# Optimization experiments

Hardware: AMD Instinct MI355X
Metric: run time of the kernel (lower is better)

## Reference

```python
import jax, jax.numpy as jnp
import numpy as np

H, KVH, DH = 16, 4, 128
EPS = 1e-8

def _rmsnorm(t, gamma):
    # normalize over last dim (dim_head)
    ms = jnp.mean(t * t, axis=-1, keepdims=True)
    return t * jax.lax.rsqrt(ms + EPS) * gamma

def setup_inputs() -> dict:
    key = jax.random.key(0)
    ks = jax.random.split(key, 5)
    d = H * DH  # 2048
    kv_d = KVH * DH  # 512
    x = jax.random.normal(ks[0], (2, 2048, d), dtype=jnp.float32)
    Wq = jax.random.normal(ks[1], (d, d), dtype=jnp.float32) * (d ** -0.5)
    Wk = jax.random.normal(ks[2], (d, kv_d), dtype=jnp.float32) * (d ** -0.5)
    Wv = jax.random.normal(ks[3], (d, kv_d), dtype=jnp.float32) * (d ** -0.5)
    Wo = jax.random.normal(ks[4], (d, d), dtype=jnp.float32) * (d ** -0.5)
    q_gamma = jnp.ones((DH,), dtype=jnp.float32)
    k_gamma = jnp.ones((DH,), dtype=jnp.float32)
    return {"x": x, "Wq": Wq, "Wk": Wk, "Wv": Wv, "Wo": Wo,
            "q_gamma": q_gamma, "k_gamma": k_gamma}

def reference(x, Wq, Wk, Wv, Wo, q_gamma, k_gamma):
    b, s, d = x.shape
    g = H // KVH  # GQA group size
    q = (x @ Wq).reshape(b, s, H, DH)
    k = (x @ Wk).reshape(b, s, KVH, DH)
    v = (x @ Wv).reshape(b, s, KVH, DH)
    # fused QK RMSNorm (per-head, over dim_head)
    q = _rmsnorm(q, q_gamma)
    k = _rmsnorm(k, k_gamma)
    # GQA: expand kv heads across query-head groups
    k = jnp.repeat(k, g, axis=2)  # [b, s, H, DH]
    v = jnp.repeat(v, g, axis=2)
    scores = jnp.einsum('bqhd,bkhd->bhqk', q, k) * (DH ** -0.5)
    causal = jnp.tril(jnp.ones((s, s), dtype=bool))
    scores = jnp.where(causal, scores, jnp.finfo(scores.dtype).min)
    attn = jax.nn.softmax(scores, axis=-1)
    out = jnp.einsum('bhqk,bkhd->bqhd', attn, v).reshape(b, s, H * DH)
    out = out @ Wo
    return out + x  # residual skip
```

## Files before the change

kernel.cpp:

```cpp
#include <hip/hip_runtime.h>

typedef unsigned short u16;
typedef __attribute__((ext_vector_type(8))) short short8;
typedef __attribute__((ext_vector_type(4))) float f32x4;

#define DEVI __device__ __forceinline__

DEVI float u2f(u16 u) {
    unsigned int x = ((unsigned int)u) << 16;
    float f; __builtin_memcpy(&f, &x, 4); return f;
}
DEVI u16 f2u(float f) {
    unsigned int x; __builtin_memcpy(&x, &f, 4);
    x = (x + 0x7fffu + ((x >> 16) & 1u)) >> 16;
    return (u16)x;
}
DEVI unsigned int fbits(float f) {
    unsigned int x; __builtin_memcpy(&x, &f, 4); return x;
}
DEVI void gld16(const u16* g, u16* ldsbase) {
    __builtin_amdgcn_global_load_lds(
        (const __attribute__((address_space(1))) unsigned int*)g,
        (__attribute__((address_space(3))) unsigned int*)ldsbase, 16, 0, 0);
}

__global__ __launch_bounds__(256) void prep(
    const float* __restrict__ x,
    const float* __restrict__ Wq, const float* __restrict__ Wk,
    const float* __restrict__ Wv, const float* __restrict__ Wo,
    u16* __restrict__ xbf, u16* __restrict__ WTqkv, u16* __restrict__ WoT)
{
    __shared__ u16 T[64 * 72];
    int id = blockIdx.x;
    const int tid = threadIdx.x;
    if (id < 4096) {
        int g = (id * 256 + tid) * 8;
        float4 a = *(const float4*)&x[g];
        float4 c = *(const float4*)&x[g + 4];
        short8 v;
        v[0]=(short)f2u(a.x); v[1]=(short)f2u(a.y); v[2]=(short)f2u(a.z); v[3]=(short)f2u(a.w);
        v[4]=(short)f2u(c.x); v[5]=(short)f2u(c.y); v[6]=(short)f2u(c.z); v[7]=(short)f2u(c.w);
        *(short8*)&xbf[g] = v;
        return;
    }
    id -= 4096;
    const float* W; u16* WT; int N, bx, by;
    if (id < 1024)      {            W = Wo; WT = WoT;   N = 2048; bx = id & 31; by = id >> 5; }
    else if (id < 2048) { id -= 1024; W = Wq; WT = WTqkv; N = 2048; bx = id & 31; by = id >> 5; }
    else if (id < 2304) { id -= 2048; W = Wk; WT = WTqkv + (size_t)2048 * 2048; N = 512; bx = id & 7; by = id >> 3; }
    else                { id -= 2304; W = Wv; WT = WTqkv + (size_t)2560 * 2048; N = 512; bx = id & 7; by = id >> 3; }
    const int K = 2048;
    const int k0 = by * 64, n0 = bx * 64;
#pragma unroll
    for (int i = 0; i < 2; ++i) {
        int c = tid + i * 256;
        int row = c >> 3, n8 = (c & 7) * 8;
        const float* src = &W[(size_t)(k0 + row) * N + n0 + n8];
#pragma unroll
        for (int j = 0; j < 8; ++j)
            T[(n8 + j) * 72 + row] = f2u(src[j]);
    }
    __syncthreads();
#pragma unroll
    for (int i = 0; i < 2; ++i) {
        int c = tid + i * 256;
        int n = c >> 3, k8 = (c & 7) * 8;
        *(short8*)&WT[(size_t)(n0 + n) * K + k0 + k8] = *(const short8*)&T[n * 72 + k8];
    }
}

__global__ __launch_bounds__(256) void gemm_lds(
    const u16* __restrict__ A, int lda,
    const u16* __restrict__ WT,
    void* __restrict__ C, int ldc, const float* __restrict__ resid, int c_f32,
    int M, int N, int K,
    const float* __restrict__ qg, const float* __restrict__ kg, int fuse_norm)
{
    __shared__ u16 As[128 * 32];
    __shared__ u16 Bs[128 * 32];
    const int tid = threadIdx.x;
    const int lane = tid & 63, w = tid >> 6;
    const int wm = w >> 1, wn = w & 1;
    const int l15 = lane & 15, quad = lane >> 4;
    const int r4 = lane >> 2, c4 = (lane & 3) * 8;
    const int m0 = blockIdx.y * 128, n0 = blockIdx.x * 128;

    f32x4 acc[4][4] = {};
    for (int k0 = 0; k0 < K; k0 += 32) {
#pragma unroll
        for (int j = 0; j < 2; ++j) {
            int row = w * 32 + j * 16;
            gld16(&WT[(size_t)(n0 + row + r4) * K + k0 + c4], &Bs[row * 32]);
            gld16(&A [(size_t)(m0 + row + r4) * lda + k0 + c4], &As[row * 32]);
        }
        __syncthreads();
        short8 a[4], b[4];
#pragma unroll
        for (int mt = 0; mt < 4; ++mt)
            a[mt] = *(const short8*)&As[(wm * 64 + mt * 16 + l15) * 32 + quad * 8];
#pragma unroll
        for (int nt = 0; nt < 4; ++nt)
            b[nt] = *(const short8*)&Bs[(wn * 64 + nt * 16 + l15) * 32 + quad * 8];
#pragma unroll
        for (int mt = 0; mt < 4; ++mt)
#pragma unroll
            for (int nt = 0; nt < 4; ++nt)
                acc[mt][nt] = __builtin_amdgcn_mfma_f32_16x16x32_bf16(a[mt], b[nt], acc[mt][nt], 0, 0, 0);
        __syncthreads();
    }

    if (fuse_norm && n0 < 2560) {
        const float* gamma = (n0 < 2048) ? qg : kg;
        float* red = (float*)As;
#pragma unroll
        for (int mt = 0; mt < 4; ++mt)
#pragma unroll
            for (int r = 0; r < 4; ++r) {
                float p = 0.f;
#pragma unroll
                for (int nt = 0; nt < 4; ++nt) p += acc[mt][nt][r] * acc[mt][nt][r];
#pragma unroll
                for (int msk = 1; msk < 16; msk <<= 1) p += __shfl_xor(p, msk);
                if (l15 == 0)
                    red[(wm * 64 + mt * 16 + quad * 4 + r) * 2 + wn] = p;
            }
        __syncthreads();
        float gv[4];
#pragma unroll
        for (int nt = 0; nt < 4; ++nt) gv[nt] = gamma[wn * 64 + nt * 16 + l15];
#pragma unroll
        for (int mt = 0; mt < 4; ++mt)
#pragma unroll
            for (int r = 0; r < 4; ++r) {
                int rl = wm * 64 + mt * 16 + quad * 4 + r;
                float m2 = red[rl * 2] + red[rl * 2 + 1];
                float sc = rsqrtf(m2 * (1.0f / 128.0f) + 1e-8f);
#pragma unroll
                for (int nt = 0; nt < 4; ++nt) acc[mt][nt][r] *= sc * gv[nt];
            }
    }

#pragma unroll
    for (int mt = 0; mt < 4; ++mt) {
#pragma unroll
        for (int r = 0; r < 4; ++r) {
            int row = m0 + wm * 64 + mt * 16 + quad * 4 + r;
#pragma unroll
            for (int nt = 0; nt < 4; ++nt) {
                int col = n0 + wn * 64 + nt * 16 + l15;
                float v = acc[mt][nt][r];
                if (resid) v += resid[(size_t)row * ldc + col];
                if (c_f32) ((float*)C)[(size_t)row * ldc + col] = v;
                else       ((u16*)C)[(size_t)row * ldc + col] = f2u(v);
            }
        }
    }
}

__global__ __launch_bounds__(256) void vtrans(
    const u16* __restrict__ qkv, u16* __restrict__ vT)
{
    __shared__ u16 T[128 * 72];
    const int tid = threadIdx.x;
    const int t0 = blockIdx.x * 64;
    const int kvh = blockIdx.y, b = blockIdx.z;
#pragma unroll
    for (int i = 0; i < 4; ++i) {
        int c = tid + i * 256;
        int tl = c >> 4, d8 = (c & 15) * 8;
        short8 v = *(const short8*)&qkv[(size_t)(b * 2048 + t0 + tl) * 3072 + 2560 + kvh * 128 + d8];
#pragma unroll
        for (int j = 0; j < 8; ++j)
            T[(d8 + j) * 72 + tl] = (u16)v[j];
    }
    __syncthreads();
#pragma unroll
    for (int i = 0; i < 4; ++i) {
        int c = tid + i * 256;
        int d = c >> 3, t8 = (c & 7) * 8;
        *(short8*)&vT[((size_t)(b * 4 + kvh) * 128 + d) * 2048 + t0 + t8] =
            *(const short8*)&T[d * 72 + t8];
    }
}

#define SWZ(row, coloff) ((coloff) ^ (((row) & 7) << 4))
__global__ __launch_bounds__(512) void attn(
    u16* __restrict__ qkv, const u16* __restrict__ vT)
{
    __shared__ u16 lds[16384];
    char* const Kb = (char*)lds;
    char* const Vb = (char*)(lds + 8192);

    const int tid = threadIdx.x, lane = tid & 63, w = tid >> 6;
    const int t = w >> 2, wq = w & 3;
    const int l15 = lane & 15, quad = lane >> 4;
    const int h = blockIdx.y, b = blockIdx.z;
    const int kvh = h >> 2;
    const int qts[2] = { (int)blockIdx.x, 31 - (int)blockIdx.x };
    const int qt = qts[t];
    const float scale = 0.08838834764831845f;

#pragma unroll
    for (int ts = 0; ts < 2; ++ts)
#pragma unroll
        for (int i = 0; i < 2; ++i) {
            int c = tid + i * 512;
            int r = c >> 4, co = (c & 15) * 16;
            short8 v = *(const short8*)&qkv[(size_t)(b * 2048 + qts[ts] * 64 + r) * 3072 + h * 128 + (c & 15) * 8];
            *(short8*)((char*)lds + ts * 16384 + r * 256 + SWZ(r, co)) = v;
        }
    __syncthreads();
    short8 qf[4];
    {
        int row = wq * 16 + l15;
#pragma unroll
        for (int ks = 0; ks < 4; ++ks)
            qf[ks] = *(const short8*)((char*)lds + t * 16384 + row * 256 + SWZ(row, ks * 64 + quad * 16));
    }
    __syncthreads();

    f32x4 o[8] = {};
    float m_ = -1e30f, l_ = 0.f;

    for (int kt = 0; kt <= qts[1]; ++kt) {
        const int kv0 = kt * 64;
#pragma unroll
        for (int i = 0; i < 2; ++i) {
            int c = tid + i * 512;
            int r = c >> 4, co = (c & 15) * 16;
            short8 v = *(const short8*)&qkv[(size_t)(b * 2048 + kv0 + r) * 3072 + 2048 + kvh * 128 + (c & 15) * 8];
            *(short8*)(Kb + r * 256 + SWZ(r, co)) = v;
        }
#pragma unroll
        for (int i = 0; i < 2; ++i) {
            int c = tid + i * 512;
            int d = c >> 3, co = (c & 7) * 16;
            short8 v = *(const short8*)&vT[((size_t)(b * 4 + kvh) * 128 + d) * 2048 + kv0 + (c & 7) * 8];
            *(short8*)(Vb + d * 128 + SWZ(d, co)) = v;
        }
        __syncthreads();

        if (kt <= qt) {
            f32x4 s[4];
#pragma unroll
            for (int nt = 0; nt < 4; ++nt) {
                f32x4 a = {};
                int row = nt * 16 + l15;
#pragma unroll
                for (int ks = 0; ks < 4; ++ks) {
                    short8 kf = *(const short8*)(Kb + row * 256 + SWZ(row, ks * 64 + quad * 16));
                    a = __builtin_amdgcn_mfma_f32_16x16x32_bf16(kf, qf[ks], a, 0, 0, 0);
                }
                s[nt] = a;
            }
            if (kt == qt) {
                int qrow = wq * 16 + l15;
#pragma unroll
                for (int nt = 0; nt < 4; ++nt)
#pragma unroll
                    for (int r = 0; r < 4; ++r) {
                        float v = s[nt][r] * scale;
                        if (nt * 16 + quad * 4 + r > qrow) v = -1e30f;
                        s[nt][r] = v;
                    }
            } else {
#pragma unroll
                for (int nt = 0; nt < 4; ++nt)
#pragma unroll
                    for (int r = 0; r < 4; ++r) s[nt][r] *= scale;
            }
            float mx = s[0][0];
#pragma unroll
            for (int nt = 0; nt < 4; ++nt)
#pragma unroll
                for (int r = 0; r < 4; ++r) mx = fmaxf(mx, s[nt][r]);
            mx = fmaxf(mx, __shfl_xor(mx, 16));
            mx = fmaxf(mx, __shfl_xor(mx, 32));
            float mn = fmaxf(m_, mx);
            float alpha = __expf(m_ - mn);
            m_ = mn;
            float sum = 0.f;
#pragma unroll
            for (int nt = 0; nt < 4; ++nt)
#pragma unroll
                for (int r = 0; r < 4; ++r) {
                    float p = __expf(s[nt][r] - mn);
                    s[nt][r] = p;
                    sum += p;
                }
            sum += __shfl_xor(sum, 16);
            sum += __shfl_xor(sum, 32);
            l_ = l_ * alpha + sum;
            unsigned int pk[4][2];
#pragma unroll
            for (int nt = 0; nt < 4; ++nt)
#pragma unroll
                for (int i = 0; i < 2; ++i)
                    pk[nt][i] = __builtin_amdgcn_perm(
                        fbits(s[nt][2 * i + 1]), fbits(s[nt][2 * i]), 0x07060302u);
            int af[2][4];
#pragma unroll
            for (int c = 0; c < 2; ++c)
#pragma unroll
                for (int d = 0; d < 4; ++d) {
                    int src = l15 + 16 * ((quad & 1) * 2 + (d >> 1));
                    int v0 = __shfl((int)pk[2 * c][d & 1], src);
                    int v1 = __shfl((int)pk[2 * c + 1][d & 1], src);
                    af[c][d] = (quad >= 2) ? v1 : v0;
                }
            union { int i4[4]; short8 s8; } ua0, ua1;
#pragma unroll
            for (int d = 0; d < 4; ++d) { ua0.i4[d] = af[0][d]; ua1.i4[d] = af[1][d]; }
#pragma unroll
            for (int r = 0; r < 4; ++r) {
                float ao = __shfl(alpha, quad * 4 + r);
#pragma unroll
                for (int nto = 0; nto < 8; ++nto) o[nto][r] *= ao;
            }
#pragma unroll
            for (int nto = 0; nto < 8; ++nto) {
                int row = nto * 16 + l15;
                const char* vb = Vb + row * 128;
                short8 bv0 = *(const short8*)(vb + SWZ(row, quad * 16));
                short8 bv1 = *(const short8*)(vb + SWZ(row, 64 + quad * 16));
                o[nto] = __builtin_amdgcn_mfma_f32_16x16x32_bf16(ua0.s8, bv0, o[nto], 0, 0, 0);
                o[nto] = __builtin_amdgcn_mfma_f32_16x16x32_bf16(ua1.s8, bv1, o[nto], 0, 0, 0);
            }
        }
        __syncthreads();
    }
    {
        float rl = 1.0f / l_;
#pragma unroll
        for (int r = 0; r < 4; ++r) {
            float inv = __shfl(rl, quad * 4 + r);
            int row = qt * 64 + wq * 16 + quad * 4 + r;
#pragma unroll
            for (int nto = 0; nto < 8; ++nto)
                qkv[(size_t)(b * 2048 + row) * 3072 + h * 128 + nto * 16 + l15] =
                    f2u(o[nto][r] * inv);
        }
    }
}

extern "C" void kernel_launch(void* const* d_in, const int* in_sizes, int n_in,
                              void* d_out, int out_size, void* d_ws, size_t ws_size,
                              hipStream_t stream) {
    const float* x  = (const float*)d_in[0];
    const float* Wq = (const float*)d_in[1];
    const float* Wk = (const float*)d_in[2];
    const float* Wv = (const float*)d_in[3];
    const float* Wo = (const float*)d_in[4];
    const float* qg = (const float*)d_in[5];
    const float* kg = (const float*)d_in[6];

    char* ws = (char*)d_ws;
    u16* WoT   = (u16*)(ws);
    u16* QKV   = (u16*)(ws + 8388608);
    u16* vT    = (u16*)(ws + 33554432);
    u16* WTqkv = (u16*)(ws + 33554432);
    u16* xbf   = (u16*)d_out;

    prep<<<dim3(6656), 256, 0, stream>>>(x, Wq, Wk, Wv, Wo, xbf, WTqkv, WoT);

    gemm_lds<<<dim3(24, 32), 256, 0, stream>>>(xbf, 2048, WTqkv, QKV, 3072,
                                               nullptr, 0, 4096, 3072, 2048,
                                               qg, kg, 1);

    vtrans<<<dim3(32, 4, 2), 256, 0, stream>>>(QKV, vT);

    attn<<<dim3(16, 16, 2), 512, 0, stream>>>(QKV, vT);

    gemm_lds<<<dim3(16, 32), 256, 0, stream>>>(QKV, 3072, WoT, d_out, 2048,
                                               x, 1, 4096, 2048, 2048,
                                               nullptr, nullptr, 0);
}
```

Baseline: 373.1 us.

## Switch attention to 32x32x16 MFMA with 4-wave blocks and lazy rescaling

Rewrites the attention kernel to use 32x32x16 bf16 MFMA tiles. Each wave now owns 32 query rows, so blocks shrink to 256 threads, Q fragments are loaded straight from global memory, and the P-to-A-operand repack needs one cross-half swap instead of many shuffles. It also skips the online-softmax rescale of the output accumulator unless the running max grows by more than a threshold. The intent is fewer MFMA issues, fewer shuffles and less rescale work per tile, at the cost of more registers per wave and fewer waves per block to hide load latency.

```diff
diff --git a/kernel.cpp b/kernel.cpp
--- a/kernel.cpp
+++ b/kernel.cpp
@@ -3,6 +3,7 @@
 typedef unsigned short u16;
 typedef __attribute__((ext_vector_type(8))) short short8;
 typedef __attribute__((ext_vector_type(4))) float f32x4;
+typedef __attribute__((ext_vector_type(16))) float f32x16;
 
 #define DEVI __device__ __forceinline__
 
@@ -17,6 +18,9 @@
 }
 DEVI unsigned int fbits(float f) {
     unsigned int x; __builtin_memcpy(&x, &f, 4); return x;
+}
+DEVI unsigned int pkbf(float lo, float hi) {
+    return __builtin_amdgcn_perm(fbits(hi), fbits(lo), 0x07060302u);
 }
 DEVI void gld16(const u16* g, u16* ldsbase) {
     __builtin_amdgcn_global_load_lds(
@@ -184,56 +188,45 @@
 }
 
 #define SWZ(row, coloff) ((coloff) ^ (((row) & 7) << 4))
-__global__ __launch_bounds__(512) void attn(
+__global__ __launch_bounds__(256) void attn(
     u16* __restrict__ qkv, const u16* __restrict__ vT)
 {
     __shared__ u16 lds[16384];
     char* const Kb = (char*)lds;
-    char* const Vb = (char*)(lds + 8192);
+    char* const Vb = (char*)lds + 16384;
 
     const int tid = threadIdx.x, lane = tid & 63, w = tid >> 6;
-    const int t = w >> 2, wq = w & 3;
-    const int l15 = lane & 15, quad = lane >> 4;
+    const int t = w >> 1, half = w & 1;
+    const int l31 = lane & 31, h2 = lane >> 5;
     const int h = blockIdx.y, b = blockIdx.z;
     const int kvh = h >> 2;
     const int qts[2] = { (int)blockIdx.x, 31 - (int)blockIdx.x };
     const int qt = qts[t];
     const float scale = 0.08838834764831845f;
 
-#pragma unroll
-    for (int ts = 0; ts < 2; ++ts)
-#pragma unroll
-        for (int i = 0; i < 2; ++i) {
-            int c = tid + i * 512;
-            int r = c >> 4, co = (c & 15) * 16;
-            short8 v = *(const short8*)&qkv[(size_t)(b * 2048 + qts[ts] * 64 + r) * 3072 + h * 128 + (c & 15) * 8];
-            *(short8*)((char*)lds + ts * 16384 + r * 256 + SWZ(r, co)) = v;
-        }
-    __syncthreads();
-    short8 qf[4];
+    short8 qf[8];
     {
-        int row = wq * 16 + l15;
-#pragma unroll
-        for (int ks = 0; ks < 4; ++ks)
-            qf[ks] = *(const short8*)((char*)lds + t * 16384 + row * 256 + SWZ(row, ks * 64 + quad * 16));
-    }
-    __syncthreads();
-
-    f32x4 o[8] = {};
+        const u16* Qg = &qkv[(size_t)(b * 2048 + qt * 64 + half * 32 + l31) * 3072 + h * 128 + h2 * 8];
+#pragma unroll
+        for (int ks = 0; ks < 8; ++ks)
+            qf[ks] = *(const short8*)&Qg[ks * 16];
+    }
+
+    f32x16 o2[4] = {};
     float m_ = -1e30f, l_ = 0.f;
 
     for (int kt = 0; kt <= qts[1]; ++kt) {
         const int kv0 = kt * 64;
 #pragma unroll
-        for (int i = 0; i < 2; ++i) {
-            int c = tid + i * 512;
+        for (int i = 0; i < 4; ++i) {
+            int c = tid + i * 256;
             int r = c >> 4, co = (c & 15) * 16;
             short8 v = *(const short8*)&qkv[(size_t)(b * 2048 + kv0 + r) * 3072 + 2048 + kvh * 128 + (c & 15) * 8];
             *(short8*)(Kb + r * 256 + SWZ(r, co)) = v;
         }
 #pragma unroll
-        for (int i = 0; i < 2; ++i) {
-            int c = tid + i * 512;
+        for (int i = 0; i < 4; ++i) {
+            int c = tid + i * 256;
             int d = c >> 3, co = (c & 7) * 16;
             short8 v = *(const short8*)&vT[((size_t)(b * 4 + kvh) * 128 + d) * 2048 + kv0 + (c & 7) * 8];
             *(short8*)(Vb + d * 128 + SWZ(d, co)) = v;
@@ -241,90 +234,91 @@
         __syncthreads();
 
         if (kt <= qt) {
-            f32x4 s[4];
-#pragma unroll
-            for (int nt = 0; nt < 4; ++nt) {
-                f32x4 a = {};
-                int row = nt * 16 + l15;
-#pragma unroll
-                for (int ks = 0; ks < 4; ++ks) {
-                    short8 kf = *(const short8*)(Kb + row * 256 + SWZ(row, ks * 64 + quad * 16));
-                    a = __builtin_amdgcn_mfma_f32_16x16x32_bf16(kf, qf[ks], a, 0, 0, 0);
+            f32x16 s2[2];
+#pragma unroll
+            for (int nt2 = 0; nt2 < 2; ++nt2) {
+                f32x16 a = {};
+                int row = nt2 * 32 + l31;
+#pragma unroll
+                for (int ks = 0; ks < 8; ++ks) {
+                    short8 kf = *(const short8*)(Kb + row * 256 + SWZ(row, ks * 32 + h2 * 16));
+                    a = __builtin_amdgcn_mfma_f32_32x32x16_bf16(kf, qf[ks], a, 0, 0, 0);
                 }
-                s[nt] = a;
+                s2[nt2] = a;
             }
             if (kt == qt) {
-                int qrow = wq * 16 + l15;
-#pragma unroll
-                for (int nt = 0; nt < 4; ++nt)
-#pragma unroll
-                    for (int r = 0; r < 4; ++r) {
-                        float v = s[nt][r] * scale;
-                        if (nt * 16 + quad * 4 + r > qrow) v = -1e30f;
-                        s[nt][r] = v;
+                int qrow = half * 32 + l31;
+#pragma unroll
+                for (int nt2 = 0; nt2 < 2; ++nt2)
+#pragma unroll
+                    for (int r = 0; r < 16; ++r) {
+                        int kvr = nt2 * 32 + (r & 3) + 8 * (r >> 2) + 4 * h2;
+                        float v = s2[nt2][r] * scale;
+                        if (kvr > qrow) v = -1e30f;
+                        s2[nt2][r] = v;
                     }
             } else {
 #pragma unroll
-                for (int nt = 0; nt < 4; ++nt)
-#pragma unroll
-                    for (int r = 0; r < 4; ++r) s[nt][r] *= scale;
-            }
-            float mx = s[0][0];
-#pragma unroll
-            for (int nt = 0; nt < 4; ++nt)
-#pragma unroll
-                for (int r = 0; r < 4; ++r) mx = fmaxf(mx, s[nt][r]);
-            mx = fmaxf(mx, __shfl_xor(mx, 16));
+                for (int nt2 = 0; nt2 < 2; ++nt2)
+#pragma unroll
+                    for (int r = 0; r < 16; ++r) s2[nt2][r] *= scale;
+            }
+            float mx = s2[0][0];
+#pragma unroll
+            for (int nt2 = 0; nt2 < 2; ++nt2)
+#pragma unroll
+                for (int r = 0; r < 16; ++r) mx = fmaxf(mx, s2[nt2][r]);
             mx = fmaxf(mx, __shfl_xor(mx, 32));
-            float mn = fmaxf(m_, mx);
-            float alpha = __expf(m_ - mn);
-            m_ = mn;
+            if (!__all(mx <= m_ + 8.0f)) {
+                float mn = fmaxf(m_, mx);
+                float alpha = __expf(m_ - mn);
+                m_ = mn;
+                l_ *= alpha;
+#pragma unroll
+                for (int r = 0; r < 16; ++r) {
+                    float ar = __shfl(alpha, (r & 3) + 8 * (r >> 2) + 4 * h2);
+#pragma unroll
+                    for (int dblk = 0; dblk < 4; ++dblk) o2[dblk][r] *= ar;
+                }
+            }
             float sum = 0.f;
 #pragma unroll
-            for (int nt = 0; nt < 4; ++nt)
-#pragma unroll
-                for (int r = 0; r < 4; ++r) {
-                    float p = __expf(s[nt][r] - mn);
-                    s[nt][r] = p;
+            for (int nt2 = 0; nt2 < 2; ++nt2)
+#pragma unroll
+                for (int r = 0; r < 16; ++r) {
+                    float p = __expf(s2[nt2][r] - m_);
+                    s2[nt2][r] = p;
                     sum += p;
                 }
-            sum += __shfl_xor(sum, 16);
             sum += __shfl_xor(sum, 32);
-            l_ = l_ * alpha + sum;
-            unsigned int pk[4][2];
-#pragma unroll
-            for (int nt = 0; nt < 4; ++nt)
-#pragma unroll
-                for (int i = 0; i < 2; ++i)
-                    pk[nt][i] = __builtin_amdgcn_perm(
-                        fbits(s[nt][2 * i + 1]), fbits(s[nt][2 * i]), 0x07060302u);
-            int af[2][4];
-#pragma unroll
-            for (int c = 0; c < 2; ++c)
-#pragma unroll
-                for (int d = 0; d < 4; ++d) {
-                    int src = l15 + 16 * ((quad & 1) * 2 + (d >> 1));
-                    int v0 = __shfl((int)pk[2 * c][d & 1], src);
-                    int v1 = __shfl((int)pk[2 * c + 1][d & 1], src);
-                    af[c][d] = (quad >= 2) ? v1 : v0;
+            l_ += sum;
+            short8 pa[4];
+#pragma unroll
+            for (int ch = 0; ch < 4; ++ch) {
+                int nt2 = ch >> 1, cc = (ch & 1) * 8;
+                unsigned int xa = pkbf(s2[nt2][cc + 0], s2[nt2][cc + 1]);
+                unsigned int xb = pkbf(s2[nt2][cc + 2], s2[nt2][cc + 3]);
+                unsigned int xc = pkbf(s2[nt2][cc + 4], s2[nt2][cc + 5]);
+                unsigned int xd = pkbf(s2[nt2][cc + 6], s2[nt2][cc + 7]);
+                unsigned int r1 = (unsigned int)__shfl_xor((int)(h2 ? xa : xc), 32);
+                unsigned int r2 = (unsigned int)__shfl_xor((int)(h2 ? xb : xd), 32);
+                union { unsigned int u[4]; short8 s8; } uu;
+                uu.u[0] = h2 ? r1 : xa;
+                uu.u[1] = h2 ? r2 : xb;
+                uu.u[2] = h2 ? xc : r1;
+                uu.u[3] = h2 ? xd : r2;
+                pa[ch] = uu.s8;
+            }
+#pragma unroll
+            for (int dblk = 0; dblk < 4; ++dblk) {
+                int row = dblk * 32 + l31;
+                f32x16 acc = o2[dblk];
+#pragma unroll
+                for (int ch = 0; ch < 4; ++ch) {
+                    short8 bv = *(const short8*)(Vb + row * 128 + SWZ(row, ch * 32 + h2 * 16));
+                    acc = __builtin_amdgcn_mfma_f32_32x32x16_bf16(pa[ch], bv, acc, 0, 0, 0);
                 }
-            union { int i4[4]; short8 s8; } ua0, ua1;
-#pragma unroll
-            for (int d = 0; d < 4; ++d) { ua0.i4[d] = af[0][d]; ua1.i4[d] = af[1][d]; }
-#pragma unroll
-            for (int r = 0; r < 4; ++r) {
-                float ao = __shfl(alpha, quad * 4 + r);
-#pragma unroll
-                for (int nto = 0; nto < 8; ++nto) o[nto][r] *= ao;
-            }
-#pragma unroll
-            for (int nto = 0; nto < 8; ++nto) {
-                int row = nto * 16 + l15;
-                const char* vb = Vb + row * 128;
-                short8 bv0 = *(const short8*)(vb + SWZ(row, quad * 16));
-                short8 bv1 = *(const short8*)(vb + SWZ(row, 64 + quad * 16));
-                o[nto] = __builtin_amdgcn_mfma_f32_16x16x32_bf16(ua0.s8, bv0, o[nto], 0, 0, 0);
-                o[nto] = __builtin_amdgcn_mfma_f32_16x16x32_bf16(ua1.s8, bv1, o[nto], 0, 0, 0);
+                o2[dblk] = acc;
             }
         }
         __syncthreads();
@@ -332,13 +326,14 @@
     {
         float rl = 1.0f / l_;
 #pragma unroll
-        for (int r = 0; r < 4; ++r) {
-            float inv = __shfl(rl, quad * 4 + r);
-            int row = qt * 64 + wq * 16 + quad * 4 + r;
-#pragma unroll
-            for (int nto = 0; nto < 8; ++nto)
-                qkv[(size_t)(b * 2048 + row) * 3072 + h * 128 + nto * 16 + l15] =
-                    f2u(o[nto][r] * inv);
+        for (int r = 0; r < 16; ++r) {
+            int qreg = (r & 3) + 8 * (r >> 2) + 4 * h2;
+            float inv = __shfl(rl, qreg);
+            int row = qt * 64 + half * 32 + qreg;
+#pragma unroll
+            for (int dblk = 0; dblk < 4; ++dblk)
+                qkv[(size_t)(b * 2048 + row) * 3072 + h * 128 + dblk * 32 + l31] =
+                    f2u(o2[dblk][r] * inv);
         }
     }
 }
@@ -369,7 +364,7 @@
 
     vtrans<<<dim3(32, 4, 2), 256, 0, stream>>>(QKV, vT);
 
-    attn<<<dim3(16, 16, 2), 512, 0, stream>>>(QKV, vT);
+    attn<<<dim3(16, 16, 2), 256, 0, stream>>>(QKV, vT);
 
     gemm_lds<<<dim3(16, 32), 256, 0, stream>>>(QKV, 3072, WoT, d_out, 2048,
                                                x, 1, 4096, 2048, 2048,
```

Result: slower. 415.4 us (+11.3%).
